# Performance work log

Hardware: AMD Instinct MI355X
Metric: run time of the kernel (lower is better)

Reference implementation:

```python
import jax, jax.numpy as jnp
import numpy as np

NUM_PROJS = 7
BLOCK_SIZE = 256   # key block size
SAMPLE_SIZE = 256  # residual sampled keys


def _gray_perm(n):
    # AngularLSH._unit_hamming_distance_array: Gray-code bucket permutation
    a = np.array([0, 1], dtype=np.int32)
    for i in range(1, n):
        a = np.concatenate([a, a[::-1] + 2 ** i])
    return a

PERM = jnp.asarray(_gray_perm(NUM_PROJS))
ENC = jnp.asarray(2 ** np.arange(NUM_PROJS), dtype=jnp.int32)


def lsh_hash(x, proj_dir):
    # sign-bit angular LSH -> Gray-code bucket id, [B,H,N]
    bits = (jnp.einsum('bhnd,dr->bhnr', x, proj_dir) > 0).astype(jnp.int32)
    return PERM[(bits * ENC).sum(-1)]


def exact_attention(q, k, v, scale, bias=None):
    s = jnp.einsum('...qd,...kd->...qk', q, k) * scale
    if bias is not None:
        s = s + bias
    lse = jax.nn.logsumexp(s, axis=-1, keepdims=True)
    attn = jnp.einsum('...qk,...kd->...qd', jnp.exp(s - lse), v)
    return attn, lse


def add_self_attentions(a1, l1, a2, l2):
    # stable online-softmax combination of two attention partials
    c = jax.nn.sigmoid(l1 - l2)  # = exp(l1)/(exp(l1)+exp(l2))
    return c * a1 + (1.0 - c) * a2, jnp.logaddexp(l1, l2)


def gather_seq(x, idx):
    # x: [B,H,N,D], idx: [B,H,S] -> [B,H,S,D]
    return jnp.take_along_axis(x, idx[..., None], axis=2)


def hyper_attention(query, key, value, proj_dir, sampled_set):
    B, H, Nq, D = query.shape
    Nk = key.shape[2]
    scale = D ** -0.5
    # --- LSH bucket sort of queries and keys (stable, matches torch.sort stable=True) ---
    q_idx = jnp.argsort(lsh_hash(query, proj_dir), axis=2, stable=True)
    k_idx = jnp.argsort(lsh_hash(key, proj_dir), axis=2, stable=True)
    q_idx_inv = jnp.argsort(q_idx, axis=2, stable=True)
    q_s = gather_seq(query, q_idx)
    k_s = gather_seq(key, k_idx)
    v_s = gather_seq(value, k_idx)
    # --- block-diagonal attention over LSH-sorted blocks ---
    nb = Nk // BLOCK_SIZE          # 32 blocks
    qbs = Nq // nb                 # query block size (== 256 here)
    attn_b, lse_b = exact_attention(
        q_s.reshape(B, H, nb, qbs, D),
        k_s.reshape(B, H, nb, BLOCK_SIZE, D),
        v_s.reshape(B, H, nb, BLOCK_SIZE, D),
        scale)
    attn_b = attn_b.reshape(B, H, Nq, D)
    lse_b = lse_b.reshape(B, H, Nq, 1)
    # --- residual: uniformly sampled keys, importance weight Nk/SAMPLE_SIZE ---
    k_sub = gather_seq(k_s, sampled_set)
    v_sub = gather_seq(v_s, sampled_set)
    q_pos = jnp.arange(Nq) // qbs                    # [Nq] query block ids
    s_blk = sampled_set // BLOCK_SIZE                # [B,H,S] sampled key block ids
    overlap = q_pos[None, None, :, None] == s_blk[:, :, None, :]  # [B,H,Nq,S]
    bias = jnp.where(overlap, jnp.finfo(query.dtype).min, 0.0).astype(query.dtype)
    attn_r, lse_r = exact_attention(q_s, k_sub, v_sub, scale, bias)
    lse_r = lse_r + jnp.asarray(np.log(Nk / SAMPLE_SIZE), lse_r.dtype)
    # --- combine partials via online LSE, then unsort queries ---
    attn, lse = add_self_attentions(attn_b, lse_b, attn_r, lse_r)
    attn = gather_seq(attn, q_idx_inv)
    return attn


def setup_inputs() -> dict:
    key = jax.random.key(0)
    kq, kk, kv, kp, ks = jax.random.split(key, 5)
    B, H, N, D = 2, 16, 8192, 64
    return {
        'query': jax.random.normal(kq, (B, H, N, D), jnp.float32),
        'key': jax.random.normal(kk, (B, H, N, D), jnp.float32),
        'value': jax.random.normal(kv, (B, H, N, D), jnp.float32),
        'proj_dir': jax.random.normal(kp, (D, NUM_PROJS), jnp.float32),
        'sampled_set': jax.random.randint(ks, (B, H, SAMPLE_SIZE), 0, N),
    }


def reference(query, key, value, proj_dir, sampled_set):
    return hyper_attention(query, key, value, proj_dir, sampled_set)
```

## Files before the change

### kernel.cpp

```cpp
#include <hip/hip_runtime.h>

#define BHX   32
#define NSEQ  8192
#define NMASK 8191
#define DIM   64
#define NPROJ 7
#define NBUCK 128
#define NBLK  32
#define QBS   256
#define SSIZE 256
#define LOG32 3.4657359027997265f
#define KPAD  72

typedef unsigned short u16;
typedef unsigned int   u32;
typedef unsigned char  u8;
typedef __attribute__((ext_vector_type(8))) short bf16x8;
typedef __attribute__((ext_vector_type(4))) float f32x4;

union B8U { u32 u[4]; bf16x8 v; };

__device__ __forceinline__ u16 f2bf(float f){
    u32 u = __float_as_uint(f);
    u32 r = u + 0x7fffu + ((u >> 16) & 1u);
    return (u16)(r >> 16);
}
__device__ __forceinline__ u32 pk2(float a, float b){
    return (u32)f2bf(a) | ((u32)f2bf(b) << 16);
}
__device__ __forceinline__ f32x4 mfma16(bf16x8 a, bf16x8 b, f32x4 c){
    return __builtin_amdgcn_mfma_f32_16x16x32_bf16(a, b, c, 0, 0, 0);
}

__global__ __launch_bounds__(256) void hash_kernel(
    const float* __restrict__ qg, const float* __restrict__ kg,
    const float* __restrict__ projg,
    u8* __restrict__ bkt)
{
    const int slab = blockIdx.x, bh = blockIdx.y, tz = blockIdx.z;
    const float* __restrict__ x = tz ? kg : qg;
    u8* __restrict__ ob = bkt + ((size_t)tz * BHX + bh) * NSEQ;

    __shared__ float projs[NPROJ][DIM];
    const int t = threadIdx.x;
    if (t < 112) {
        #pragma unroll
        for (int u = 0; u < 4; u++) {
            int e = t * 4 + u;
            projs[e % NPROJ][e / NPROJ] = projg[e];
        }
    }
    __syncthreads();

    const size_t bhN = (size_t)bh * NSEQ;
    #pragma unroll
    for (int j = 0; j < 4; j++) {
        int n = slab * 1024 + j * 256 + t;
        const float4* row = (const float4*)(x + (bhN + n) * DIM);
        float dot[NPROJ];
        #pragma unroll
        for (int r = 0; r < NPROJ; r++) dot[r] = 0.0f;
        #pragma unroll
        for (int c = 0; c < 16; c++) {
            float4 w = row[c];
            float f[4] = {w.x, w.y, w.z, w.w};
            #pragma unroll
            for (int u = 0; u < 4; u++) {
                float xv = f[u];
                int d = c * 4 + u;
                #pragma unroll
                for (int r = 0; r < NPROJ; r++) dot[r] += xv * projs[r][d];
            }
        }
        int code = 0;
        #pragma unroll
        for (int r = 0; r < NPROJ; r++) code |= (dot[r] > 0.0f ? 1 : 0) << r;
        ob[n] = (u8)(code ^ (code >> 1));
    }
}

__global__ __launch_bounds__(256) void sort_kernel(
    const u8* __restrict__ bkt,
    u16* __restrict__ qidx, u16* __restrict__ kidx)
{
    const int bh = blockIdx.x, tz = blockIdx.y;
    const u8* __restrict__ ib = bkt + ((size_t)tz * BHX + bh) * NSEQ;
    u16* __restrict__ idx = (tz ? kidx : qidx) + (size_t)bh * NSEQ;

    __shared__ u8  lb[NSEQ];
    __shared__ u16 hist[NBUCK][258];
    __shared__ int base[NBUCK];
    __shared__ int tot[NBUCK];

    const int t = threadIdx.x;
    {
        const uint4* src = (const uint4*)ib;
        uint4* dst = (uint4*)lb;
        dst[t] = src[t];
        dst[256 + t] = src[256 + t];
    }
    u32* hz = (u32*)&hist[0][0];
    for (int z = t; z < (NBUCK * 258) / 2; z += 256) hz[z] = 0u;
    __syncthreads();

    #pragma unroll 4
    for (int i = 0; i < 32; i++) hist[lb[t * 32 + i]][t]++;
    __syncthreads();

    if (t < NBUCK) {
        u32 run = 0;
        for (int c = 0; c < 256; c++) {
            u32 v = hist[t][c];
            hist[t][c] = (u16)run;
            run += v;
        }
        tot[t] = (int)run;
    }
    __syncthreads();
    if (t == 0) {
        int run = 0;
        for (int b = 0; b < NBUCK; b++) { base[b] = run; run += tot[b]; }
    }
    __syncthreads();

    #pragma unroll 4
    for (int i = 0; i < 32; i++) {
        int n = t * 32 + i;
        int b = lb[n];
        int pos = base[b] + hist[b][t];
        hist[b][t]++;
        idx[pos] = (u16)n;
    }
}

__global__ __launch_bounds__(256, 2) void attn_mfma(
    const float* __restrict__ qg, const float* __restrict__ kg,
    const float* __restrict__ vg,
    const u16* __restrict__ qidx, const u16* __restrict__ kidx,
    const int* __restrict__ samp,
    float* __restrict__ outg)
{
    __shared__ u16  Ks[64 * KPAD];
    __shared__ u16  Vt[64 * KPAD];
    __shared__ u16  Ps[4 * 64 * KPAD];
    __shared__ float addv[64];

    const int qb = blockIdx.x, bh = blockIdx.y, t = threadIdx.x;
    const int w = t >> 6, lane = t & 63, c = lane & 15, g = lane >> 4;
    const size_t bhN = (size_t)bh * NSEQ;

    int qi[4];
    bf16x8 qf[4][2];
    #pragma unroll
    for (int qt = 0; qt < 4; qt++) {
        qi[qt] = ((int)qidx[bhN + qb * QBS + w * 64 + qt * 16 + c]) & NMASK;
        const float* qr = qg + (bhN + (size_t)qi[qt]) * DIM;
        #pragma unroll
        for (int dk = 0; dk < 2; dk++) {
            int d0 = dk * 32 + g * 8;
            float4 x = *(const float4*)(qr + d0);
            float4 y = *(const float4*)(qr + d0 + 4);
            B8U f;
            f.u[0] = pk2(x.x * 0.125f, x.y * 0.125f);
            f.u[1] = pk2(x.z * 0.125f, x.w * 0.125f);
            f.u[2] = pk2(y.x * 0.125f, y.y * 0.125f);
            f.u[3] = pk2(y.z * 0.125f, y.w * 0.125f);
            qf[qt][dk] = f.v;
        }
    }

    f32x4 O[4][4];
    #pragma unroll
    for (int dt = 0; dt < 4; dt++)
        #pragma unroll
        for (int qt = 0; qt < 4; qt++) O[dt][qt] = (f32x4)0.0f;
    float m[4] = {-1e30f, -1e30f, -1e30f, -1e30f};
    float l[4] = {0.0f, 0.0f, 0.0f, 0.0f};

    for (int cc = 0; cc < 8; cc++) {
        __syncthreads();
        {
            int s = t >> 2, seg = (t & 3) * 16;
            int grow; float add;
            if (cc < 4) {
                grow = ((int)kidx[bhN + qb * QBS + cc * 64 + s]) & NMASK;
                add  = 0.0f;
            } else {
                int sidx = samp[bh * SSIZE + (cc - 4) * 64 + s] & NMASK;
                grow = ((int)kidx[bhN + sidx]) & NMASK;
                add  = ((sidx >> 8) == qb) ? -1e30f : LOG32;
            }
            const float4* kr = (const float4*)(kg + (bhN + (size_t)grow) * DIM + seg);
            float4 a = kr[0], b = kr[1], e = kr[2], d = kr[3];
            u32* dst = (u32*)&Ks[s * KPAD + seg];
            dst[0] = pk2(a.x, a.y); dst[1] = pk2(a.z, a.w);
            dst[2] = pk2(b.x, b.y); dst[3] = pk2(b.z, b.w);
            dst[4] = pk2(e.x, e.y); dst[5] = pk2(e.z, e.w);
            dst[6] = pk2(d.x, d.y); dst[7] = pk2(d.z, d.w);
            const float4* vr = (const float4*)(vg + (bhN + (size_t)grow) * DIM + seg);
            float4 va = vr[0], vb = vr[1], vc = vr[2], vd = vr[3];
            float vv[16] = {va.x, va.y, va.z, va.w, vb.x, vb.y, vb.z, vb.w,
                            vc.x, vc.y, vc.z, vc.w, vd.x, vd.y, vd.z, vd.w};
            #pragma unroll
            for (int i = 0; i < 16; i++) Vt[(seg + i) * KPAD + s] = f2bf(vv[i]);
            if ((t & 3) == 0) addv[s] = add;
        }
        __syncthreads();

        f32x4 addn[4];
        #pragma unroll
        for (int kt = 0; kt < 4; kt++)
            addn[kt] = *(const f32x4*)&addv[kt * 16 + g * 4];

        bf16x8 ka[4][2];
        #pragma unroll
        for (int kt = 0; kt < 4; kt++)
            #pragma unroll
            for (int dk = 0; dk < 2; dk++)
                ka[kt][dk] = *(const bf16x8*)&Ks[(kt * 16 + c) * KPAD + dk * 32 + g * 8];

        #pragma unroll
        for (int qt = 0; qt < 4; qt++) {
            f32x4 S[4];
            #pragma unroll
            for (int kt = 0; kt < 4; kt++) {
                S[kt] = (f32x4)0.0f;
                S[kt] = mfma16(ka[kt][0], qf[qt][0], S[kt]);
                S[kt] = mfma16(ka[kt][1], qf[qt][1], S[kt]);
            }
            float cmax = -1e30f;
            #pragma unroll
            for (int kt = 0; kt < 4; kt++)
                #pragma unroll
                for (int r = 0; r < 4; r++)
                    cmax = fmaxf(cmax, S[kt][r] + addn[kt][r]);
            cmax = fmaxf(cmax, __shfl_xor(cmax, 16));
            cmax = fmaxf(cmax, __shfl_xor(cmax, 32));
            float mnew  = fmaxf(m[qt], cmax);
            float alpha = __expf(m[qt] - mnew);
            m[qt] = mnew;
            float lsum = 0.0f;
            u16* prow = &Ps[(size_t)(w * 64 + qt * 16 + c) * KPAD];
            #pragma unroll
            for (int kt = 0; kt < 4; kt++) {
                float p0 = __expf(S[kt][0] + addn[kt][0] - mnew);
                float p1 = __expf(S[kt][1] + addn[kt][1] - mnew);
                float p2 = __expf(S[kt][2] + addn[kt][2] - mnew);
                float p3 = __expf(S[kt][3] + addn[kt][3] - mnew);
                lsum += (p0 + p1) + (p2 + p3);
                u32* pw = (u32*)&prow[kt * 16 + g * 4];
                pw[0] = pk2(p0, p1);
                pw[1] = pk2(p2, p3);
            }
            lsum += __shfl_xor(lsum, 16);
            lsum += __shfl_xor(lsum, 32);
            l[qt] = l[qt] * alpha + lsum;
            #pragma unroll
            for (int dt = 0; dt < 4; dt++) O[dt][qt] *= alpha;
        }

        #pragma unroll
        for (int kk = 0; kk < 2; kk++) {
            bf16x8 vfr[4], pfr[4];
            #pragma unroll
            for (int dt = 0; dt < 4; dt++)
                vfr[dt] = *(const bf16x8*)&Vt[(dt * 16 + c) * KPAD + kk * 32 + g * 8];
            #pragma unroll
            for (int qt = 0; qt < 4; qt++)
                pfr[qt] = *(const bf16x8*)&Ps[(size_t)(w * 64 + qt * 16 + c) * KPAD + kk * 32 + g * 8];
            #pragma unroll
            for (int dt = 0; dt < 4; dt++)
                #pragma unroll
                for (int qt = 0; qt < 4; qt++)
                    O[dt][qt] = mfma16(vfr[dt], pfr[qt], O[dt][qt]);
        }
    }

    #pragma unroll
    for (int qt = 0; qt < 4; qt++) {
        float inv = 1.0f / fmaxf(l[qt], 1e-30f);
        float* orow = outg + (bhN + (size_t)qi[qt]) * DIM;
        #pragma unroll
        for (int dt = 0; dt < 4; dt++) {
            f32x4 o = O[dt][qt] * inv;
            *(f32x4*)(orow + dt * 16 + g * 4) = o;
        }
    }
}

extern "C" void kernel_launch(void* const* d_in, const int* in_sizes, int n_in,
                              void* d_out, int out_size, void* d_ws, size_t ws_size,
                              hipStream_t stream)
{
    const float* qg   = (const float*)d_in[0];
    const float* kg   = (const float*)d_in[1];
    const float* vg   = (const float*)d_in[2];
    const float* pg   = (const float*)d_in[3];
    const int*   samp = (const int*)d_in[4];
    float* outg = (float*)d_out;

    u16* qidx = (u16*)d_ws;
    u16* kidx = qidx + BHX * NSEQ;
    u8*  bkt  = (u8*)(kidx + BHX * NSEQ);

    hipLaunchKernelGGL(hash_kernel, dim3(8, BHX, 2), dim3(256), 0, stream,
                       qg, kg, pg, bkt);
    hipLaunchKernelGGL(sort_kernel, dim3(BHX, 2), dim3(256), 0, stream,
                       bkt, qidx, kidx);
    hipLaunchKernelGGL(attn_mfma, dim3(NBLK, BHX), dim3(256), 0, stream,
                       qg, kg, vg, qidx, kidx, samp, outg);
}
```

Before: 314.2 us.

## Pre-gather transposed bf16 V blocks and stream K fragments directly in attention

Adds a gather_v kernel that writes each sorted key block's V, transposed and converted to bf16, into workspace, plus a sampled_prep kernel that does the same for the 256 residual-sampled keys and precomputes their indices and block ids. A new attention kernel loads K fragments straight from global memory into registers and reads V fragments from the pre-transposed buffers, so the K/V shared-memory staging is gone and only the P tile stays in LDS. The hash kernel now stages rows through a shared-memory tile so its global loads are coalesced. The new path costs extra launches and about 32 MB of workspace traffic, and it falls back to the old attention kernel when the workspace is too small.

```diff
diff --git a/kernel.cpp b/kernel.cpp
--- a/kernel.cpp
+++ b/kernel.cpp
@@ -32,6 +32,8 @@
     return __builtin_amdgcn_mfma_f32_16x16x32_bf16(a, b, c, 0, 0, 0);
 }
 
+#define VTB(bh, kb, d, key) (((((size_t)(bh) * NBLK + (kb)) * DIM + (d)) * 256) + (key))
+
 __global__ __launch_bounds__(256) void hash_kernel(
     const float* __restrict__ qg, const float* __restrict__ kg,
     const float* __restrict__ projg,
@@ -41,7 +43,9 @@
     const float* __restrict__ x = tz ? kg : qg;
     u8* __restrict__ ob = bkt + ((size_t)tz * BHX + bh) * NSEQ;
 
+    __shared__ float tile[256][68];
     __shared__ float projs[NPROJ][DIM];
+
     const int t = threadIdx.x;
     if (t < 112) {
         #pragma unroll
@@ -50,19 +54,25 @@
             projs[e % NPROJ][e / NPROJ] = projg[e];
         }
     }
-    __syncthreads();
 
     const size_t bhN = (size_t)bh * NSEQ;
-    #pragma unroll
-    for (int j = 0; j < 4; j++) {
-        int n = slab * 1024 + j * 256 + t;
-        const float4* row = (const float4*)(x + (bhN + n) * DIM);
+    for (int T = 0; T < 4; T++) {
+        __syncthreads();
+        const float* gsrc = x + (bhN + slab * 1024 + T * 256) * DIM;
+        #pragma unroll
+        for (int i = 0; i < 16; i++) {
+            int fd  = i * 1024 + t * 4;
+            int row = fd >> 6, col = fd & 63;
+            *(float4*)&tile[row][col] = *(const float4*)(gsrc + fd);
+        }
+        __syncthreads();
+
         float dot[NPROJ];
         #pragma unroll
         for (int r = 0; r < NPROJ; r++) dot[r] = 0.0f;
         #pragma unroll
         for (int c = 0; c < 16; c++) {
-            float4 w = row[c];
+            float4 w = *(const float4*)&tile[t][c * 4];
             float f[4] = {w.x, w.y, w.z, w.w};
             #pragma unroll
             for (int u = 0; u < 4; u++) {
@@ -75,7 +85,7 @@
         int code = 0;
         #pragma unroll
         for (int r = 0; r < NPROJ; r++) code |= (dot[r] > 0.0f ? 1 : 0) << r;
-        ob[n] = (u8)(code ^ (code >> 1));
+        ob[slab * 1024 + T * 256 + t] = (u8)(code ^ (code >> 1));
     }
 }
 
@@ -130,6 +140,200 @@
         int pos = base[b] + hist[b][t];
         hist[b][t]++;
         idx[pos] = (u16)n;
+    }
+}
+
+__global__ __launch_bounds__(256) void gather_v(
+    const float* __restrict__ vg, const u16* __restrict__ kidx,
+    u16* __restrict__ vt)
+{
+    const int kb = blockIdx.x, bh = blockIdx.y, t = threadIdx.x;
+    const size_t bhN = (size_t)bh * NSEQ;
+    const int grow = ((int)kidx[bhN + kb * 256 + t]) & NMASK;
+    const float4* vr = (const float4*)(vg + (bhN + (size_t)grow) * DIM);
+    float v[DIM];
+    #pragma unroll
+    for (int c = 0; c < 16; c++) {
+        float4 w = vr[c];
+        v[c * 4 + 0] = w.x; v[c * 4 + 1] = w.y;
+        v[c * 4 + 2] = w.z; v[c * 4 + 3] = w.w;
+    }
+    #pragma unroll
+    for (int d = 0; d < DIM; d++)
+        vt[VTB(bh, kb, d, t)] = f2bf(v[d]);
+}
+
+__global__ __launch_bounds__(256) void sampled_prep(
+    const float* __restrict__ vg, const u16* __restrict__ kidx,
+    const int* __restrict__ samp,
+    u16* __restrict__ skidx, u8* __restrict__ sblk, u16* __restrict__ svt)
+{
+    const int bh = blockIdx.x, t = threadIdx.x;
+    const size_t bhN = (size_t)bh * NSEQ;
+    const int sidx = samp[bh * SSIZE + t] & NMASK;
+    const int grow = ((int)kidx[bhN + sidx]) & NMASK;
+    skidx[bh * SSIZE + t] = (u16)grow;
+    sblk[bh * SSIZE + t]  = (u8)(sidx >> 8);
+    const float4* vr = (const float4*)(vg + (bhN + (size_t)grow) * DIM);
+    float v[DIM];
+    #pragma unroll
+    for (int c = 0; c < 16; c++) {
+        float4 w = vr[c];
+        v[c * 4 + 0] = w.x; v[c * 4 + 1] = w.y;
+        v[c * 4 + 2] = w.z; v[c * 4 + 3] = w.w;
+    }
+    #pragma unroll
+    for (int d = 0; d < DIM; d++)
+        svt[((size_t)bh * DIM + d) * 256 + t] = f2bf(v[d]);
+}
+
+__global__ __launch_bounds__(256, 2) void attn_fast(
+    const float* __restrict__ qg, const float* __restrict__ kg,
+    const u16* __restrict__ vt, const u16* __restrict__ svt,
+    const u16* __restrict__ qidx, const u16* __restrict__ kidx,
+    const u16* __restrict__ skidx, const u8* __restrict__ sblk,
+    float* __restrict__ outg)
+{
+    __shared__ u16 Ps[4 * 64 * KPAD];
+
+    const int qb = blockIdx.x, bh = blockIdx.y, t = threadIdx.x;
+    const int w = t >> 6, lane = t & 63, c = lane & 15, g = lane >> 4;
+    const size_t bhN = (size_t)bh * NSEQ;
+
+    int qi[4];
+    bf16x8 qf[4][2];
+    #pragma unroll
+    for (int qt = 0; qt < 4; qt++) {
+        qi[qt] = ((int)qidx[bhN + qb * QBS + w * 64 + qt * 16 + c]) & NMASK;
+        const float* qr = qg + (bhN + (size_t)qi[qt]) * DIM;
+        #pragma unroll
+        for (int dk = 0; dk < 2; dk++) {
+            int d0 = dk * 32 + g * 8;
+            float4 x = *(const float4*)(qr + d0);
+            float4 y = *(const float4*)(qr + d0 + 4);
+            B8U f;
+            f.u[0] = pk2(x.x * 0.125f, x.y * 0.125f);
+            f.u[1] = pk2(x.z * 0.125f, x.w * 0.125f);
+            f.u[2] = pk2(y.x * 0.125f, y.y * 0.125f);
+            f.u[3] = pk2(y.z * 0.125f, y.w * 0.125f);
+            qf[qt][dk] = f.v;
+        }
+    }
+
+    f32x4 O[4][4];
+    #pragma unroll
+    for (int dt = 0; dt < 4; dt++)
+        #pragma unroll
+        for (int qt = 0; qt < 4; qt++) O[dt][qt] = (f32x4)0.0f;
+    float m[4] = {-1e30f, -1e30f, -1e30f, -1e30f};
+    float l[4] = {0.0f, 0.0f, 0.0f, 0.0f};
+
+    for (int cc = 0; cc < 8; cc++) {
+        const bool blk = (cc < 4);
+        const u16* kri = blk ? &kidx[bhN + qb * QBS + cc * 64]
+                             : &skidx[bh * SSIZE + (cc - 4) * 64];
+
+        bf16x8 ka[4][2];
+        #pragma unroll
+        for (int kt = 0; kt < 4; kt++) {
+            int r = ((int)kri[kt * 16 + c]) & NMASK;
+            const float* kr = kg + (bhN + (size_t)r) * DIM;
+            #pragma unroll
+            for (int dk = 0; dk < 2; dk++) {
+                int d0 = dk * 32 + g * 8;
+                float4 x = *(const float4*)(kr + d0);
+                float4 y = *(const float4*)(kr + d0 + 4);
+                B8U f;
+                f.u[0] = pk2(x.x, x.y);
+                f.u[1] = pk2(x.z, x.w);
+                f.u[2] = pk2(y.x, y.y);
+                f.u[3] = pk2(y.z, y.w);
+                ka[kt][dk] = f.v;
+            }
+        }
+
+        f32x4 addn[4];
+        if (blk) {
+            #pragma unroll
+            for (int kt = 0; kt < 4; kt++) addn[kt] = (f32x4)0.0f;
+        } else {
+            #pragma unroll
+            for (int kt = 0; kt < 4; kt++) {
+                u32 sb4 = *(const u32*)&sblk[bh * SSIZE + (cc - 4) * 64 + kt * 16 + g * 4];
+                #pragma unroll
+                for (int r = 0; r < 4; r++)
+                    addn[kt][r] = (((sb4 >> (8 * r)) & 255u) == (u32)qb) ? -1e30f : LOG32;
+            }
+        }
+
+        #pragma unroll
+        for (int qt = 0; qt < 4; qt++) {
+            f32x4 S[4];
+            #pragma unroll
+            for (int kt = 0; kt < 4; kt++) {
+                S[kt] = (f32x4)0.0f;
+                S[kt] = mfma16(ka[kt][0], qf[qt][0], S[kt]);
+                S[kt] = mfma16(ka[kt][1], qf[qt][1], S[kt]);
+            }
+            float cmax = -1e30f;
+            #pragma unroll
+            for (int kt = 0; kt < 4; kt++)
+                #pragma unroll
+                for (int r = 0; r < 4; r++)
+                    cmax = fmaxf(cmax, S[kt][r] + addn[kt][r]);
+            cmax = fmaxf(cmax, __shfl_xor(cmax, 16));
+            cmax = fmaxf(cmax, __shfl_xor(cmax, 32));
+            float mnew  = fmaxf(m[qt], cmax);
+            float alpha = __expf(m[qt] - mnew);
+            m[qt] = mnew;
+            float lsum = 0.0f;
+            u16* prow = &Ps[(size_t)(w * 64 + qt * 16 + c) * KPAD];
+            #pragma unroll
+            for (int kt = 0; kt < 4; kt++) {
+                float p0 = __expf(S[kt][0] + addn[kt][0] - mnew);
+                float p1 = __expf(S[kt][1] + addn[kt][1] - mnew);
+                float p2 = __expf(S[kt][2] + addn[kt][2] - mnew);
+                float p3 = __expf(S[kt][3] + addn[kt][3] - mnew);
+                lsum += (p0 + p1) + (p2 + p3);
+                u32* pw = (u32*)&prow[kt * 16 + g * 4];
+                pw[0] = pk2(p0, p1);
+                pw[1] = pk2(p2, p3);
+            }
+            lsum += __shfl_xor(lsum, 16);
+            lsum += __shfl_xor(lsum, 32);
+            l[qt] = l[qt] * alpha + lsum;
+            #pragma unroll
+            for (int dt = 0; dt < 4; dt++) O[dt][qt] *= alpha;
+        }
+
+        const u16* vtb = blk ? &vt[VTB(bh, qb, 0, cc * 64)]
+                             : &svt[((size_t)bh * DIM) * 256 + (cc - 4) * 64];
+        #pragma unroll
+        for (int kk = 0; kk < 2; kk++) {
+            bf16x8 vfr[4], pfr[4];
+            #pragma unroll
+            for (int dt = 0; dt < 4; dt++)
+                vfr[dt] = *(const bf16x8*)&vtb[(size_t)(dt * 16 + c) * 256 + kk * 32 + g * 8];
+            #pragma unroll
+            for (int qt = 0; qt < 4; qt++)
+                pfr[qt] = *(const bf16x8*)&Ps[(size_t)(w * 64 + qt * 16 + c) * KPAD + kk * 32 + g * 8];
+            #pragma unroll
+            for (int dt = 0; dt < 4; dt++)
+                #pragma unroll
+                for (int qt = 0; qt < 4; qt++)
+                    O[dt][qt] = mfma16(vfr[dt], pfr[qt], O[dt][qt]);
+        }
+    }
+
+    #pragma unroll
+    for (int qt = 0; qt < 4; qt++) {
+        float inv = 1.0f / fmaxf(l[qt], 1e-30f);
+        float* orow = outg + (bhN + (size_t)qi[qt]) * DIM;
+        #pragma unroll
+        for (int dt = 0; dt < 4; dt++) {
+            f32x4 o = O[dt][qt] * inv;
+            *(f32x4*)(orow + dt * 16 + g * 4) = o;
+        }
     }
 }
 
@@ -299,14 +503,31 @@
     const int*   samp = (const int*)d_in[4];
     float* outg = (float*)d_out;
 
-    u16* qidx = (u16*)d_ws;
-    u16* kidx = qidx + BHX * NSEQ;
-    u8*  bkt  = (u8*)(kidx + BHX * NSEQ);
+    char* ws = (char*)d_ws;
+    size_t off = 0;
+    u16* qidx  = (u16*)(ws + off); off += (size_t)BHX * NSEQ * 2;
+    u16* kidx  = (u16*)(ws + off); off += (size_t)BHX * NSEQ * 2;
+    u8*  bkt   = (u8*) (ws + off); off += (size_t)2 * BHX * NSEQ;
+    u16* skidx = (u16*)(ws + off); off += (size_t)BHX * SSIZE * 2;
+    u8*  sblk  = (u8*) (ws + off); off += (size_t)BHX * SSIZE;
+    off = (off + 255) & ~(size_t)255;
+    u16* svt   = (u16*)(ws + off); off += (size_t)BHX * DIM * 256 * 2;
+    u16* vt    = (u16*)(ws + off); off += (size_t)BHX * NBLK * DIM * 256 * 2;
+    const bool fast = (ws_size >= off);
 
     hipLaunchKernelGGL(hash_kernel, dim3(8, BHX, 2), dim3(256), 0, stream,
                        qg, kg, pg, bkt);
     hipLaunchKernelGGL(sort_kernel, dim3(BHX, 2), dim3(256), 0, stream,
                        bkt, qidx, kidx);
-    hipLaunchKernelGGL(attn_mfma, dim3(NBLK, BHX), dim3(256), 0, stream,
-                       qg, kg, vg, qidx, kidx, samp, outg);
-}
+    if (fast) {
+        hipLaunchKernelGGL(gather_v, dim3(NBLK, BHX), dim3(256), 0, stream,
+                           vg, kidx, vt);
+        hipLaunchKernelGGL(sampled_prep, dim3(BHX), dim3(256), 0, stream,
+                           vg, kidx, samp, skidx, sblk, svt);
+        hipLaunchKernelGGL(attn_fast, dim3(NBLK, BHX), dim3(256), 0, stream,
+                           qg, kg, vt, svt, qidx, kidx, skidx, sblk, outg);
+    } else {
+        hipLaunchKernelGGL(attn_mfma, dim3(NBLK, BHX), dim3(256), 0, stream,
+                           qg, kg, vg, qidx, kidx, samp, outg);
+    }
+}
```

New measurement: 406.0 us. +29.2%, slower.
